# Kernel optimization log

Hardware: AMD Instinct MI355X
Metric: run time of the kernel (lower is better)

The kernel has to match this reference:

```python
import jax, jax.numpy as jnp
import numpy as np

NEAR = 0.0
SCENE_SCALE = 1.0
OPACITY_THRESHOLD = 0.01
EARLY_TERM = 1e-4
N_RAYS = 4096
N_SAMPLES = 256
GRID = 128
FEAT = 64
HID = 128
RGB_HID = 64


def mip360_contract(c):
    # Mip-NeRF 360 scene contraction; safe norm avoids NaN grads in the unused branch.
    norm = jnp.linalg.norm(c, axis=-1, keepdims=True)
    safe = jnp.maximum(norm, 1e-12)
    return jnp.where(norm <= 1.0, c, (2.0 - 1.0 / safe) * c / safe) / 2.0


def unbounded_stepping(near, uniform_range, n):
    ts = jnp.linspace(0.0, 1.0 - 1.0 / (n + 2), n + 1)
    ts = jnp.where(ts < 0.5, 2.0 * ts, 1.0 / (2.0 - 2.0 * ts)) * uniform_range + near
    return ts[:-1], ts[1:] - ts[:-1]


def grid_sample_3d(grid, coords):
    # torch F.grid_sample bilinear, align_corners=False, zeros padding.
    # grid [D,H,W]; coords [...,3] = (x,y,z) with x->W, y->H, z->D, in [-1,1].
    D, H, W = grid.shape
    x, y, z = coords[..., 0], coords[..., 1], coords[..., 2]
    ix = ((x + 1.0) * W - 1.0) * 0.5
    iy = ((y + 1.0) * H - 1.0) * 0.5
    iz = ((z + 1.0) * D - 1.0) * 0.5
    ix0, iy0, iz0 = jnp.floor(ix), jnp.floor(iy), jnp.floor(iz)
    fx, fy, fz = ix - ix0, iy - iy0, iz - iz0
    out = jnp.zeros(x.shape, grid.dtype)
    for dz in (0, 1):
        for dy in (0, 1):
            for dx in (0, 1):
                cx, cy, cz = ix0 + dx, iy0 + dy, iz0 + dz
                w = (fx if dx else 1.0 - fx) * (fy if dy else 1.0 - fy) * (fz if dz else 1.0 - fz)
                valid = (cx >= 0) & (cx < W) & (cy >= 0) & (cy < H) & (cz >= 0) & (cz < D)
                g = grid[jnp.clip(cz, 0, D - 1).astype(jnp.int32),
                         jnp.clip(cy, 0, H - 1).astype(jnp.int32),
                         jnp.clip(cx, 0, W - 1).astype(jnp.int32)]
                out = out + jnp.where(valid, w * g, 0.0)
    return out


def setup_inputs() -> dict:
    key = jax.random.key(0)
    ks = jax.random.split(key, 8)
    rays_o = jax.random.normal(ks[0], (N_RAYS, 3), jnp.float32) * 0.3
    rd = jax.random.normal(ks[1], (N_RAYS, 3), jnp.float32)
    rays_d = rd / jnp.linalg.norm(rd, axis=-1, keepdims=True)
    grid = jax.random.uniform(ks[2], (GRID, GRID, GRID), jnp.float32)
    lin = lambda k, fan_in, shape: jax.random.normal(k, shape, jnp.float32) / np.sqrt(fan_in).astype(np.float32)
    return dict(
        rays_o=rays_o, rays_d=rays_d, grid=grid,
        f_w1=lin(ks[3], 3, (3, HID)), f_b1=jnp.zeros((HID,), jnp.float32),
        f_w2=lin(ks[4], HID, (HID, FEAT)), f_b2=jnp.zeros((FEAT,), jnp.float32),
        s_w=lin(ks[5], FEAT, (FEAT, 1)), s_b=jnp.zeros((1,), jnp.float32),
        r_w1=lin(ks[6], FEAT + 3, (FEAT + 3, RGB_HID)), r_b1=jnp.zeros((RGB_HID,), jnp.float32),
        r_w2=lin(ks[7], RGB_HID, (RGB_HID, 3)), r_b2=jnp.zeros((3,), jnp.float32),
        n_samples=N_SAMPLES,
    )


def reference(rays_o, rays_d, grid, f_w1, f_b1, f_w2, f_b2, s_w, s_b, r_w1, r_b1, r_w2, r_b2, n_samples):
    n_rays = rays_o.shape[0]
    t, dist = unbounded_stepping(NEAR, SCENE_SCALE, n_samples)               # [S], [S]
    samples = rays_o[:, None, :] + rays_d[:, None, :] * t[None, :, None]     # [R,S,3]
    samples = mip360_contract(samples)
    occ = grid_sample_3d(grid, samples)                                      # [R,S]
    mask = occ > OPACITY_THRESHOLD
    # feature module (dense compute, masked write as in samples_features[mask] = ...)
    feat = jax.nn.relu(samples @ f_w1 + f_b1) @ f_w2 + f_b2                  # [R,S,F]
    feat = jnp.where(mask[..., None], feat, 0.0)
    sigma = jnp.where(mask, jax.nn.softplus(feat @ s_w + s_b)[..., 0], 0.0)  # [R,S]
    a = -sigma * dist[None, :]
    trans = jnp.concatenate(
        [jnp.ones((n_rays, 1), a.dtype), jnp.exp(jnp.cumsum(a, axis=1))[:, :-1]], axis=1)
    weights = trans * (1.0 - jnp.exp(a))                                     # [R,S]
    mask2 = mask & (trans > EARLY_TERM)
    dirs = jnp.broadcast_to(rays_d[:, None, :], samples.shape)
    h = jax.nn.relu(jnp.concatenate([feat, dirs], axis=-1) @ r_w1 + r_b1)
    rgb = jax.nn.sigmoid(h @ r_w2 + r_b2) * weights[..., None]
    rgb = jnp.where(mask2[..., None], rgb, 0.0)
    return rgb.sum(axis=1)                                                   # [R,3]
```

## Files before the change

kernel.cpp:

```cpp
#include <hip/hip_runtime.h>
#include <hip/hip_bf16.h>
#include <math.h>
#include <stdint.h>

#define S    256
#define GN   128

typedef __attribute__((ext_vector_type(8))) short  short8;
typedef __attribute__((ext_vector_type(4))) float  floatx4;
typedef __attribute__((ext_vector_type(2))) float  float2v;

#define WS_BHI 0
#define WS_RW1 16384
#define WS_B2S 24576
#define WS_WS2 24592
#define WS_W1P 25104
#define WS_W2E 27152

__device__ __forceinline__ unsigned short bf16_rtne(float f) {
    uint32_t u = __builtin_bit_cast(uint32_t, f);
    uint32_t r = (u + 0x7fffu + ((u >> 16) & 1u)) >> 16;
    return (unsigned short)r;
}
__device__ __forceinline__ uint32_t cvt_pk_bf16(float a, float b) {
    float2 hh; hh.x = a; hh.y = b;
    __hip_bfloat162 pk = __float22bfloat162_rn(hh);
    uint32_t u; __builtin_memcpy(&u, &pk, 4);
    return u;
}

__global__ __launch_bounds__(256)
void nerf_prep(const float* __restrict__ f_w1, const float* __restrict__ f_b1,
               const float* __restrict__ f_w2, const float* __restrict__ f_b2,
               const float* __restrict__ s_w,  const float* __restrict__ s_b,
               const float* __restrict__ r_w1, const float* __restrict__ r_w2,
               unsigned char* __restrict__ ws)
{
    const int tid = threadIdx.x;
    if (tid < 128) {
        float acc = 0.0f;
        for (int n = 0; n < 64; ++n) acc += f_w2[tid * 64 + n] * s_w[n];
        ((float*)(ws + WS_WS2))[tid] = acc;
    } else if (tid == 128) {
        float acc = s_b[0];
        for (int n = 0; n < 64; ++n) acc += f_b2[n] * s_w[n];
        *(float*)(ws + WS_B2S) = acc;
    }
    {
        float* w1pk = (float*)(ws + WS_W1P);
        for (int pp = tid; pp < 64; pp += 256) {
            int k0 = 2 * pp, k1 = 2 * pp + 1;
            w1pk[pp * 8 + 0] = f_w1[k0];       w1pk[pp * 8 + 1] = f_w1[k1];
            w1pk[pp * 8 + 2] = f_w1[128 + k0]; w1pk[pp * 8 + 3] = f_w1[128 + k1];
            w1pk[pp * 8 + 4] = f_w1[256 + k0]; w1pk[pp * 8 + 5] = f_w1[256 + k1];
            w1pk[pp * 8 + 6] = f_b1[k0];       w1pk[pp * 8 + 7] = f_b1[k1];
        }
    }

    unsigned short* bhi = (unsigned short*)(ws + WS_BHI);
    for (int i = tid; i < 8192; i += 256) {
        int j = i & 7, L = (i >> 3) & 63, g = i >> 9;
        int tn = g & 3, kc = g >> 2;
        int q = L >> 4, cc = L & 15;
        int k = kc * 32 + q * 8 + j;
        bhi[i] = bf16_rtne(f_w2[k * 64 + tn * 16 + cc]);
    }
    unsigned short* rw = (unsigned short*)(ws + WS_RW1);
    for (int i = tid; i < 4096; i += 256) {
        int j = i & 7, L = (i >> 3) & 63, g = i >> 9;
        int tn = g & 3, ks = g >> 2;
        int q = L >> 4, cc = L & 15;
        int k = ks * 32 + q * 8 + j;
        rw[i] = bf16_rtne(r_w1[k * 64 + tn * 16 + cc]);
    }
    unsigned short* w2e = (unsigned short*)(ws + WS_W2E);
    for (int i = tid; i < 1024; i += 256) {
        int j = i & 7, L = (i >> 3) & 63, kf = i >> 9;
        int q = L >> 4, ch = L & 15;
        int k = kf * 32 + q * 8 + j;
        w2e[i] = (ch < 3) ? bf16_rtne(r_w2[k * 3 + ch]) : (unsigned short)0;
    }
}

__global__ __launch_bounds__(256, 4)
void nerf_mfma(const float* __restrict__ rays_o,
               const float* __restrict__ rays_d,
               const float* __restrict__ grid,
               const float* __restrict__ f_b2,
               const float* __restrict__ r_w1,
               const float* __restrict__ r_b1,
               const float* __restrict__ r_b2,
               const unsigned char* __restrict__ ws,
               float* __restrict__ out)
{
    __shared__ unsigned short fh[256 * 64];
    __shared__ float w1p[512];
    __shared__ float ws2L[128];
    __shared__ float aLds[S];
    __shared__ float maskLds[S];
    __shared__ float distLds[S];
    __shared__ float sWaveSum[4];
    __shared__ float sPart[4][3];

    const int tid   = threadIdx.x;
    const int ray   = blockIdx.x;
    const int lane  = tid & 63;
    const int wv    = tid >> 6;
    const int q     = lane >> 4;
    const int c     = lane & 15;
    const int mbase = wv * 64;

    if (tid < 128) {
        ((float4*)w1p)[tid] = ((const float4*)(ws + WS_W1P))[tid];
        ws2L[tid] = ((const float*)(ws + WS_WS2))[tid];
    }

    const float stop = 1.0f - 1.0f / (float)(S + 2);
    const float step = stop / (float)S;
    float u0 = (float)tid * step;
    float u1 = (float)(tid + 1) * step;
    float t    = (u0 < 0.5f) ? 2.0f * u0 : 1.0f / (2.0f - 2.0f * u0);
    float tn_  = (u1 < 0.5f) ? 2.0f * u1 : 1.0f / (2.0f - 2.0f * u1);
    float dist = tn_ - t;

    float ox = rays_o[ray * 3 + 0], oy = rays_o[ray * 3 + 1], oz = rays_o[ray * 3 + 2];
    float dxv = rays_d[ray * 3 + 0], dyv = rays_d[ray * 3 + 1], dzv = rays_d[ray * 3 + 2];

    float px = ox + dxv * t, py = oy + dyv * t, pz = oz + dzv * t;
    float nrm = sqrtf(px * px + py * py + pz * pz);
    float scale = (nrm <= 1.0f) ? 0.5f : (2.0f - 1.0f / nrm) / nrm * 0.5f;
    float cx = px * scale, cy = py * scale, cz = pz * scale;

    float ix = ((cx + 1.0f) * (float)GN - 1.0f) * 0.5f;
    float iy = ((cy + 1.0f) * (float)GN - 1.0f) * 0.5f;
    float iz = ((cz + 1.0f) * (float)GN - 1.0f) * 0.5f;
    float fx0 = floorf(ix), fy0 = floorf(iy), fz0 = floorf(iz);
    float fx = ix - fx0, fy = iy - fy0, fz = iz - fz0;
    int x0 = (int)fx0, y0 = (int)fy0, z0 = (int)fz0;

    float occ = 0.0f;
    #pragma unroll
    for (int dzc = 0; dzc < 2; ++dzc)
    #pragma unroll
    for (int dyc = 0; dyc < 2; ++dyc)
    #pragma unroll
    for (int dxc = 0; dxc < 2; ++dxc) {
        int xc = x0 + dxc, yc = y0 + dyc, zc = z0 + dzc;
        float w = (dxc ? fx : 1.0f - fx) * (dyc ? fy : 1.0f - fy) * (dzc ? fz : 1.0f - fz);
        if (xc >= 0 && xc < GN && yc >= 0 && yc < GN && zc >= 0 && zc < GN)
            occ += w * grid[(zc * GN + yc) * GN + xc];
    }
    bool maskA = occ > 0.01f;
    maskLds[tid] = maskA ? 1.0f : 0.0f;
    distLds[tid] = dist;

    float cxs[4], cys[4], czs[4];
    #pragma unroll
    for (int tm = 0; tm < 4; ++tm) {
        int src = tm * 16 + c;
        cxs[tm] = __shfl(cx, src, 64);
        cys[tm] = __shfl(cy, src, 64);
        czs[tm] = __shfl(cz, src, 64);
    }
    __syncthreads();

    const unsigned short* __restrict__ bhiP = (const unsigned short*)(ws + WS_BHI);
    float sig[4];

    #pragma unroll 1
    for (int ph = 0; ph < 2; ++ph) {
        floatx4 acc[2][4];
        {
            float b2v[4];
            #pragma unroll
            for (int tn = 0; tn < 4; ++tn) b2v[tn] = f_b2[tn * 16 + c];
            #pragma unroll
            for (int tm = 0; tm < 2; ++tm)
                #pragma unroll
                for (int tn = 0; tn < 4; ++tn) {
                    floatx4 v; v[0] = b2v[tn]; v[1] = b2v[tn]; v[2] = b2v[tn]; v[3] = b2v[tn];
                    acc[tm][tn] = v;
                }
        }
        float2v sig2[2];
        sig2[0][0] = 0.0f; sig2[0][1] = 0.0f;
        sig2[1][0] = 0.0f; sig2[1][1] = 0.0f;

        #pragma unroll 2
        for (int kc = 0; kc < 4; ++kc) {
            const int k0  = kc * 32 + q * 8;
            const int pp0 = kc * 16 + q * 4;
            const float4* __restrict__ w1q4 = (const float4*)&w1p[pp0 * 8];
            float ws2r[8];
            *(float4*)(ws2r)     = *(const float4*)&ws2L[k0];
            *(float4*)(ws2r + 4) = *(const float4*)&ws2L[k0 + 4];

            uint32_t packed[2][4];
            #pragma unroll
            for (int p = 0; p < 4; ++p) {
                float4 q0 = w1q4[2 * p];
                float4 q1 = w1q4[2 * p + 1];
                float2v wx2 = {q0.x, q0.y};
                float2v wy2 = {q0.z, q0.w};
                float2v wz2 = {q1.x, q1.y};
                float2v bb2 = {q1.z, q1.w};
                float2v wsp = {ws2r[2 * p], ws2r[2 * p + 1]};
                #pragma unroll
                for (int tm = 0; tm < 2; ++tm) {
                    int tg = ph * 2 + tm;
                    float2v h2 = bb2;
                    h2 = __builtin_elementwise_fma((float2v){cxs[tg], cxs[tg]}, wx2, h2);
                    h2 = __builtin_elementwise_fma((float2v){cys[tg], cys[tg]}, wy2, h2);
                    h2 = __builtin_elementwise_fma((float2v){czs[tg], czs[tg]}, wz2, h2);
                    h2 = __builtin_elementwise_max(h2, (float2v){0.0f, 0.0f});
                    sig2[tm] = __builtin_elementwise_fma(h2, wsp, sig2[tm]);
                    packed[tm][p] = cvt_pk_bf16(h2[0], h2[1]);
                }
            }
            short8 Ah[2];
            #pragma unroll
            for (int tm = 0; tm < 2; ++tm) {
                uint4 v4 = {packed[tm][0], packed[tm][1], packed[tm][2], packed[tm][3]};
                Ah[tm] = __builtin_bit_cast(short8, v4);
            }
            const int bbase = (kc * 4) * 512 + lane * 8;
            #pragma unroll
            for (int tn = 0; tn < 4; ++tn) {
                short8 bh = *(const short8*)(bhiP + bbase + tn * 512);
                #pragma unroll
                for (int tm = 0; tm < 2; ++tm)
                    acc[tm][tn] = __builtin_amdgcn_mfma_f32_16x16x32_bf16(Ah[tm], bh, acc[tm][tn], 0, 0, 0);
            }
        }

        #pragma unroll
        for (int tm = 0; tm < 2; ++tm)
            #pragma unroll
            for (int tn = 0; tn < 4; ++tn)
                #pragma unroll
                for (int pr = 0; pr < 2; ++pr) {
                    uint32_t u = cvt_pk_bf16(acc[tm][tn][2 * pr], acc[tm][tn][2 * pr + 1]);
                    int n  = tn * 16 + c;
                    int m0 = mbase + (ph * 2 + tm) * 16 + q * 4 + 2 * pr;
                    int m1 = m0 + 1;
                    int i0 = m0 * 64 + (((n >> 3) ^ (m0 & 7)) << 3) + (n & 7);
                    int i1 = m1 * 64 + (((n >> 3) ^ (m1 & 7)) << 3) + (n & 7);
                    fh[i0] = (unsigned short)u;
                    fh[i1] = (unsigned short)(u >> 16);
                }
        #pragma unroll
        for (int tm = 0; tm < 2; ++tm) {
            float s = sig2[tm][0] + sig2[tm][1];
            s += __shfl_xor(s, 16);
            s += __shfl_xor(s, 32);
            sig[ph * 2 + tm] = s;
        }
    }

    {
        float b2s = *(const float*)(ws + WS_B2S);
        if (q == 0) {
            #pragma unroll
            for (int tm = 0; tm < 4; ++tm) {
                int m = mbase + tm * 16 + c;
                float sa = sig[tm] + b2s;
                float sg = (maskLds[m] > 0.5f)
                         ? (fmaxf(sa, 0.0f) + __logf(1.0f + __expf(-fabsf(sa)))) : 0.0f;
                aLds[m] = -sg * distLds[m];
            }
        }
    }
    __builtin_amdgcn_wave_barrier();

    float hd[4];
    #pragma unroll
    for (int tn = 0; tn < 4; ++tn) {
        int n = tn * 16 + c;
        hd[tn] = r_b1[n] + dxv * r_w1[64 * 64 + n] + dyv * r_w1[65 * 64 + n] + dzv * r_w1[66 * 64 + n];
    }

    float av = aLds[tid];
    float v = av;
    #pragma unroll
    for (int off = 1; off < 64; off <<= 1) {
        float u2 = __shfl_up(v, off);
        if (lane >= off) v += u2;
    }
    if (lane == 63) sWaveSum[wv] = v;
    __syncthreads();
    float basev = 0.0f;
    #pragma unroll
    for (int w = 0; w < 4; ++w) basev += (w < wv) ? sWaveSum[w] : 0.0f;
    float excl = __shfl_up(v, 1);
    if (lane == 0) excl = 0.0f;
    float cum    = basev + excl;
    float trans  = __expf(cum);
    float weight = trans * (1.0f - __expf(av));
    bool  mask2  = maskA && (trans > 1e-4f);

    const unsigned short* __restrict__ rwP = (const unsigned short*)(ws + WS_RW1);

    #pragma unroll 1
    for (int ph = 0; ph < 2; ++ph) {
        short8 afr[2][2];
        #pragma unroll
        for (int tm = 0; tm < 2; ++tm)
            #pragma unroll
            for (int ks = 0; ks < 2; ++ks) {
                int m = mbase + (ph * 2 + tm) * 16 + c;
                int gl = ks * 4 + q;
                afr[tm][ks] = *(const short8*)&fh[m * 64 + ((gl ^ (m & 7)) << 3)];
            }

        floatx4 acc[2][4];
        #pragma unroll
        for (int tm = 0; tm < 2; ++tm)
            #pragma unroll
            for (int tn = 0; tn < 4; ++tn) {
                floatx4 z; z[0] = 0.0f; z[1] = 0.0f; z[2] = 0.0f; z[3] = 0.0f;
                acc[tm][tn] = z;
            }
        #pragma unroll
        for (int ks = 0; ks < 2; ++ks)
            #pragma unroll
            for (int tn = 0; tn < 4; ++tn) {
                short8 rb = *(const short8*)(rwP + ((ks * 4 + tn) * 64 + lane) * 8);
                #pragma unroll
                for (int tm = 0; tm < 2; ++tm)
                    acc[tm][tn] = __builtin_amdgcn_mfma_f32_16x16x32_bf16(afr[tm][ks], rb, acc[tm][tn], 0, 0, 0);
            }

        __builtin_amdgcn_wave_barrier();
        #pragma unroll
        for (int tm = 0; tm < 2; ++tm)
            #pragma unroll
            for (int tn = 0; tn < 4; ++tn)
                #pragma unroll
                for (int pr = 0; pr < 2; ++pr) {
                    float2v a2 = {acc[tm][tn][2 * pr], acc[tm][tn][2 * pr + 1]};
                    a2 = a2 + (float2v){hd[tn], hd[tn]};
                    a2 = __builtin_elementwise_max(a2, (float2v){0.0f, 0.0f});
                    uint32_t u = cvt_pk_bf16(a2[0], a2[1]);
                    int n  = tn * 16 + c;
                    int m0 = mbase + (ph * 2 + tm) * 16 + q * 4 + 2 * pr;
                    int m1 = m0 + 1;
                    int i0 = m0 * 64 + (((n >> 3) ^ (m0 & 7)) << 3) + (n & 7);
                    int i1 = m1 * 64 + (((n >> 3) ^ (m1 & 7)) << 3) + (n & 7);
                    fh[i0] = (unsigned short)u;
                    fh[i1] = (unsigned short)(u >> 16);
                }
    }
    __builtin_amdgcn_wave_barrier();

    aLds[tid] = mask2 ? weight : 0.0f;
    __builtin_amdgcn_wave_barrier();

    const unsigned short* __restrict__ w2eP = (const unsigned short*)(ws + WS_W2E);
    short8 w2f[2];
    w2f[0] = *(const short8*)(w2eP + (0 * 64 + lane) * 8);
    w2f[1] = *(const short8*)(w2eP + (1 * 64 + lane) * 8);

    floatx4 eacc[4];
    #pragma unroll
    for (int tn = 0; tn < 4; ++tn) {
        floatx4 z; z[0] = 0.0f; z[1] = 0.0f; z[2] = 0.0f; z[3] = 0.0f;
        eacc[tn] = z;
    }
    #pragma unroll
    for (int kf = 0; kf < 2; ++kf)
        #pragma unroll
        for (int tn = 0; tn < 4; ++tn) {
            int m = mbase + tn * 16 + c;
            int gl = kf * 4 + q;
            short8 hb = *(const short8*)&fh[m * 64 + ((gl ^ (m & 7)) << 3)];
            eacc[tn] = __builtin_amdgcn_mfma_f32_16x16x32_bf16(w2f[kf], hb, eacc[tn], 0, 0, 0);
        }

    float r = 0.0f, g = 0.0f, b = 0.0f;
    if (q == 0) {
        float rb0 = r_b2[0], rb1 = r_b2[1], rb2v = r_b2[2];
        #pragma unroll
        for (int tn = 0; tn < 4; ++tn) {
            int m = mbase + tn * 16 + c;
            float wgt = aLds[m];
            r += wgt / (1.0f + __expf(-(eacc[tn][0] + rb0)));
            g += wgt / (1.0f + __expf(-(eacc[tn][1] + rb1)));
            b += wgt / (1.0f + __expf(-(eacc[tn][2] + rb2v)));
        }
    }
    #pragma unroll
    for (int off = 8; off > 0; off >>= 1) {
        r += __shfl_xor(r, off);
        g += __shfl_xor(g, off);
        b += __shfl_xor(b, off);
    }
    if (lane == 0) { sPart[wv][0] = r; sPart[wv][1] = g; sPart[wv][2] = b; }
    __syncthreads();
    if (tid == 0) {
        out[ray * 3 + 0] = sPart[0][0] + sPart[1][0] + sPart[2][0] + sPart[3][0];
        out[ray * 3 + 1] = sPart[0][1] + sPart[1][1] + sPart[2][1] + sPart[3][1];
        out[ray * 3 + 2] = sPart[0][2] + sPart[1][2] + sPart[2][2] + sPart[3][2];
    }
}

extern "C" void kernel_launch(void* const* d_in, const int* in_sizes, int n_in,
                              void* d_out, int out_size, void* d_ws, size_t ws_size,
                              hipStream_t stream) {
    const int n_rays = in_sizes[0] / 3;
    nerf_prep<<<1, 256, 0, stream>>>(
        (const float*)d_in[3], (const float*)d_in[4], (const float*)d_in[5],
        (const float*)d_in[6], (const float*)d_in[7], (const float*)d_in[8],
        (const float*)d_in[9], (const float*)d_in[11], (unsigned char*)d_ws);
    nerf_mfma<<<n_rays, 256, 0, stream>>>(
        (const float*)d_in[0],  (const float*)d_in[1],  (const float*)d_in[2],
        (const float*)d_in[6],  (const float*)d_in[9],  (const float*)d_in[10],
        (const float*)d_in[12],
        (const unsigned char*)d_ws, (float*)d_out);
}
```

Measured before the change: 176.6 us.

## Replace LDS staging with shuffles, branchless trilinear gather, hoist weight loads

Removes the aLds/maskLds/distLds shared arrays and computes the softplus/alpha per thread using register selects, so those LDS round-trips disappear. Per-sample weights are gathered with lane shuffles instead. The trilinear gather becomes branchless, with clamped indices and zeroed weights for out-of-range corners. The bf16 store index math is simplified to a constant delta, and the f_b2 and r_w1 fragment loads are hoisted out of the phase loops. In exchange, the hoisted fragments raise register pressure under launch_bounds(256,4).

```diff
diff --git a/kernel.cpp b/kernel.cpp
--- a/kernel.cpp
+++ b/kernel.cpp
@@ -96,9 +96,6 @@
     __shared__ unsigned short fh[256 * 64];
     __shared__ float w1p[512];
     __shared__ float ws2L[128];
-    __shared__ float aLds[S];
-    __shared__ float maskLds[S];
-    __shared__ float distLds[S];
     __shared__ float sWaveSum[4];
     __shared__ float sPart[4][3];
 
@@ -137,6 +134,16 @@
     float fx0 = floorf(ix), fy0 = floorf(iy), fz0 = floorf(iz);
     float fx = ix - fx0, fy = iy - fy0, fz = iz - fz0;
     int x0 = (int)fx0, y0 = (int)fy0, z0 = (int)fz0;
+    int x1 = x0 + 1, y1 = y0 + 1, z1 = z0 + 1;
+
+    float wxv[2], wyv[2], wzv[2];
+    wxv[0] = (x0 >= 0) ? (1.0f - fx) : 0.0f;  wxv[1] = (x1 < GN) ? fx : 0.0f;
+    wyv[0] = (y0 >= 0) ? (1.0f - fy) : 0.0f;  wyv[1] = (y1 < GN) ? fy : 0.0f;
+    wzv[0] = (z0 >= 0) ? (1.0f - fz) : 0.0f;  wzv[1] = (z1 < GN) ? fz : 0.0f;
+    int xc[2], yb[2], zb[2];
+    xc[0] = (x0 < 0) ? 0 : x0;              xc[1] = (x1 > GN - 1) ? GN - 1 : x1;
+    yb[0] = ((y0 < 0) ? 0 : y0) * GN;       yb[1] = ((y1 > GN - 1) ? GN - 1 : y1) * GN;
+    zb[0] = ((z0 < 0) ? 0 : z0) * (GN*GN);  zb[1] = ((z1 > GN - 1) ? GN - 1 : z1) * (GN*GN);
 
     float occ = 0.0f;
     #pragma unroll
@@ -145,14 +152,10 @@
     for (int dyc = 0; dyc < 2; ++dyc)
     #pragma unroll
     for (int dxc = 0; dxc < 2; ++dxc) {
-        int xc = x0 + dxc, yc = y0 + dyc, zc = z0 + dzc;
-        float w = (dxc ? fx : 1.0f - fx) * (dyc ? fy : 1.0f - fy) * (dzc ? fz : 1.0f - fz);
-        if (xc >= 0 && xc < GN && yc >= 0 && yc < GN && zc >= 0 && zc < GN)
-            occ += w * grid[(zc * GN + yc) * GN + xc];
+        float w = (wxv[dxc] * wyv[dyc]) * wzv[dzc];
+        occ += w * grid[zb[dzc] + yb[dyc] + xc[dxc]];
     }
     bool maskA = occ > 0.01f;
-    maskLds[tid] = maskA ? 1.0f : 0.0f;
-    distLds[tid] = dist;
 
     float cxs[4], cys[4], czs[4];
     #pragma unroll
@@ -166,22 +169,20 @@
 
     const unsigned short* __restrict__ bhiP = (const unsigned short*)(ws + WS_BHI);
     float sig[4];
+    float b2v[4];
+    #pragma unroll
+    for (int tn = 0; tn < 4; ++tn) b2v[tn] = f_b2[tn * 16 + c];
 
     #pragma unroll 1
     for (int ph = 0; ph < 2; ++ph) {
         floatx4 acc[2][4];
-        {
-            float b2v[4];
-            #pragma unroll
-            for (int tn = 0; tn < 4; ++tn) b2v[tn] = f_b2[tn * 16 + c];
-            #pragma unroll
-            for (int tm = 0; tm < 2; ++tm)
-                #pragma unroll
-                for (int tn = 0; tn < 4; ++tn) {
-                    floatx4 v; v[0] = b2v[tn]; v[1] = b2v[tn]; v[2] = b2v[tn]; v[3] = b2v[tn];
-                    acc[tm][tn] = v;
-                }
-        }
+        #pragma unroll
+        for (int tm = 0; tm < 2; ++tm)
+            #pragma unroll
+            for (int tn = 0; tn < 4; ++tn) {
+                floatx4 v; v[0] = b2v[tn]; v[1] = b2v[tn]; v[2] = b2v[tn]; v[3] = b2v[tn];
+                acc[tm][tn] = v;
+            }
         float2v sig2[2];
         sig2[0][0] = 0.0f; sig2[0][1] = 0.0f;
         sig2[1][0] = 0.0f; sig2[1][1] = 0.0f;
@@ -233,6 +234,7 @@
             }
         }
 
+        const int d01 = 72 - ((c >> 3) << 4);
         #pragma unroll
         for (int tm = 0; tm < 2; ++tm)
             #pragma unroll
@@ -240,13 +242,10 @@
                 #pragma unroll
                 for (int pr = 0; pr < 2; ++pr) {
                     uint32_t u = cvt_pk_bf16(acc[tm][tn][2 * pr], acc[tm][tn][2 * pr + 1]);
-                    int n  = tn * 16 + c;
                     int m0 = mbase + (ph * 2 + tm) * 16 + q * 4 + 2 * pr;
-                    int m1 = m0 + 1;
-                    int i0 = m0 * 64 + (((n >> 3) ^ (m0 & 7)) << 3) + (n & 7);
-                    int i1 = m1 * 64 + (((n >> 3) ^ (m1 & 7)) << 3) + (n & 7);
-                    fh[i0] = (unsigned short)u;
-                    fh[i1] = (unsigned short)(u >> 16);
+                    int i0 = m0 * 64 + c + (((tn * 2) ^ (m0 & 7)) << 3);
+                    fh[i0]       = (unsigned short)u;
+                    fh[i0 + d01] = (unsigned short)(u >> 16);
                 }
         #pragma unroll
         for (int tm = 0; tm < 2; ++tm) {
@@ -257,20 +256,16 @@
         }
     }
 
+    float av;
     {
         float b2s = *(const float*)(ws + WS_B2S);
-        if (q == 0) {
-            #pragma unroll
-            for (int tm = 0; tm < 4; ++tm) {
-                int m = mbase + tm * 16 + c;
-                float sa = sig[tm] + b2s;
-                float sg = (maskLds[m] > 0.5f)
-                         ? (fmaxf(sa, 0.0f) + __logf(1.0f + __expf(-fabsf(sa)))) : 0.0f;
-                aLds[m] = -sg * distLds[m];
-            }
-        }
-    }
-    __builtin_amdgcn_wave_barrier();
+        float s01  = (q & 1) ? sig[1] : sig[0];
+        float s23  = (q & 1) ? sig[3] : sig[2];
+        float sigq = (q & 2) ? s23 : s01;
+        float sa = sigq + b2s;
+        float sg = maskA ? (fmaxf(sa, 0.0f) + __logf(1.0f + __expf(-fabsf(sa)))) : 0.0f;
+        av = -sg * dist;
+    }
 
     float hd[4];
     #pragma unroll
@@ -279,7 +274,6 @@
         hd[tn] = r_b1[n] + dxv * r_w1[64 * 64 + n] + dyv * r_w1[65 * 64 + n] + dzv * r_w1[66 * 64 + n];
     }
 
-    float av = aLds[tid];
     float v = av;
     #pragma unroll
     for (int off = 1; off < 64; off <<= 1) {
@@ -299,6 +293,14 @@
     bool  mask2  = maskA && (trans > 1e-4f);
 
     const unsigned short* __restrict__ rwP = (const unsigned short*)(ws + WS_RW1);
+    short8 rbv[2][4];
+    #pragma unroll
+    for (int ks = 0; ks < 2; ++ks)
+        #pragma unroll
+        for (int tn = 0; tn < 4; ++tn)
+            rbv[ks][tn] = *(const short8*)(rwP + ((ks * 4 + tn) * 64 + lane) * 8);
+
+    const int d01 = 72 - ((c >> 3) << 4);
 
     #pragma unroll 1
     for (int ph = 0; ph < 2; ++ph) {
@@ -323,12 +325,10 @@
         #pragma unroll
         for (int ks = 0; ks < 2; ++ks)
             #pragma unroll
-            for (int tn = 0; tn < 4; ++tn) {
-                short8 rb = *(const short8*)(rwP + ((ks * 4 + tn) * 64 + lane) * 8);
+            for (int tn = 0; tn < 4; ++tn)
                 #pragma unroll
                 for (int tm = 0; tm < 2; ++tm)
-                    acc[tm][tn] = __builtin_amdgcn_mfma_f32_16x16x32_bf16(afr[tm][ks], rb, acc[tm][tn], 0, 0, 0);
-            }
+                    acc[tm][tn] = __builtin_amdgcn_mfma_f32_16x16x32_bf16(afr[tm][ks], rbv[ks][tn], acc[tm][tn], 0, 0, 0);
 
         __builtin_amdgcn_wave_barrier();
         #pragma unroll
@@ -341,19 +341,18 @@
                     a2 = a2 + (float2v){hd[tn], hd[tn]};
                     a2 = __builtin_elementwise_max(a2, (float2v){0.0f, 0.0f});
                     uint32_t u = cvt_pk_bf16(a2[0], a2[1]);
-                    int n  = tn * 16 + c;
                     int m0 = mbase + (ph * 2 + tm) * 16 + q * 4 + 2 * pr;
-                    int m1 = m0 + 1;
-                    int i0 = m0 * 64 + (((n >> 3) ^ (m0 & 7)) << 3) + (n & 7);
-                    int i1 = m1 * 64 + (((n >> 3) ^ (m1 & 7)) << 3) + (n & 7);
-                    fh[i0] = (unsigned short)u;
-                    fh[i1] = (unsigned short)(u >> 16);
+                    int i0 = m0 * 64 + c + (((tn * 2) ^ (m0 & 7)) << 3);
+                    fh[i0]       = (unsigned short)u;
+                    fh[i0 + d01] = (unsigned short)(u >> 16);
                 }
     }
     __builtin_amdgcn_wave_barrier();
 
-    aLds[tid] = mask2 ? weight : 0.0f;
-    __builtin_amdgcn_wave_barrier();
+    float wm = mask2 ? weight : 0.0f;
+    float wgt[4];
+    #pragma unroll
+    for (int tn = 0; tn < 4; ++tn) wgt[tn] = __shfl(wm, tn * 16 + c, 64);
 
     const unsigned short* __restrict__ w2eP = (const unsigned short*)(ws + WS_W2E);
     short8 w2f[2];
@@ -381,11 +380,10 @@
         float rb0 = r_b2[0], rb1 = r_b2[1], rb2v = r_b2[2];
         #pragma unroll
         for (int tn = 0; tn < 4; ++tn) {
-            int m = mbase + tn * 16 + c;
-            float wgt = aLds[m];
-            r += wgt / (1.0f + __expf(-(eacc[tn][0] + rb0)));
-            g += wgt / (1.0f + __expf(-(eacc[tn][1] + rb1)));
-            b += wgt / (1.0f + __expf(-(eacc[tn][2] + rb2v)));
+            float wgtv = wgt[tn];
+            r += wgtv / (1.0f + __expf(-(eacc[tn][0] + rb0)));
+            g += wgtv / (1.0f + __expf(-(eacc[tn][1] + rb1)));
+            b += wgtv / (1.0f + __expf(-(eacc[tn][2] + rb2v)));
         }
     }
     #pragma unroll
```

Result: slower. 197.3 us (+11.7%).
